# Optimization experiments

Hardware: AMD Instinct MI355X
Metric: run time of the kernel (lower is better)

Reference implementation:

```python
import jax, jax.numpy as jnp
import numpy as np

N = 100000
E = 800000
IN_DIM = 128
HID = 32   # out_channels per head
HEADS = 4
OUT_DIM = 16


def _lin_init(key, fan_in, fan_out):
    k1, k2 = jax.random.split(key)
    bound = 1.0 / np.sqrt(fan_in)
    W = jax.random.uniform(k1, (fan_in, fan_out), minval=-bound, maxval=bound, dtype=jnp.float32)
    b = jax.random.uniform(k2, (fan_out,), minval=-bound, maxval=bound, dtype=jnp.float32)
    return W, b


def setup_inputs() -> dict:
    key = jax.random.key(0)
    keys = jax.random.split(key, 12)
    x = jax.random.normal(keys[0], (N, IN_DIM), dtype=jnp.float32)
    edge_index = jax.random.randint(keys[1], (2, E), 0, N, dtype=jnp.int32)
    inp = {"x": x, "edge_index": edge_index}
    in_dims = [IN_DIM, HID]
    ki = 2
    for l in range(2):
        d_in = in_dims[l]
        Wq, bq = _lin_init(keys[ki], d_in, HEADS * HID); ki += 1
        Wk, bk = _lin_init(keys[ki], d_in, HEADS * HID); ki += 1
        Wv, bv = _lin_init(keys[ki], d_in, HEADS * HID); ki += 1
        Ws, bs = _lin_init(keys[ki], d_in, HID); ki += 1
        inp.update({f"l{l}_Wq": Wq, f"l{l}_bq": bq, f"l{l}_Wk": Wk, f"l{l}_bk": bk,
                    f"l{l}_Wv": Wv, f"l{l}_bv": bv, f"l{l}_Ws": Ws, f"l{l}_bs": bs})
    Wout, bout = _lin_init(keys[ki], HID, OUT_DIM)
    inp["Wout"] = Wout
    inp["bout"] = bout
    return inp


def transformer_conv(x, src, dst, Wq, bq, Wk, bk, Wv, bv, Ws, bs):
    n = x.shape[0]
    q = (x @ Wq + bq).reshape(n, HEADS, HID)  # [N,H,C]
    k = (x @ Wk + bk).reshape(n, HEADS, HID)
    v = (x @ Wv + bv).reshape(n, HEADS, HID)
    scale = 1.0 / np.sqrt(HID)
    # per-edge attention logits over destination neighborhoods
    alpha = jnp.einsum('ehc,ehc->eh', q[dst], k[src]) * scale  # [E,H]
    m = jax.ops.segment_max(alpha, dst, num_segments=n)        # [N,H]
    p = jnp.exp(alpha - m[dst])
    s = jax.ops.segment_sum(p, dst, num_segments=n)            # [N,H]
    a = p / s[dst]                                             # [E,H]
    msg = a[:, :, None] * v[src]                               # [E,H,C]
    agg = jax.ops.segment_sum(msg, dst, num_segments=n)        # [N,H,C]
    # concat=False semantics: mean over heads, plus root/skip linear
    return agg.mean(axis=1) + (x @ Ws + bs)


def reference(x, edge_index,
              l0_Wq, l0_bq, l0_Wk, l0_bk, l0_Wv, l0_bv, l0_Ws, l0_bs,
              l1_Wq, l1_bq, l1_Wk, l1_bk, l1_Wv, l1_bv, l1_Ws, l1_bs,
              Wout, bout):
    src, dst = edge_index[0], edge_index[1]
    h = transformer_conv(x, src, dst, l0_Wq, l0_bq, l0_Wk, l0_bk, l0_Wv, l0_bv, l0_Ws, l0_bs)
    h = jax.nn.relu(h)
    h = transformer_conv(h, src, dst, l1_Wq, l1_bq, l1_Wk, l1_bk, l1_Wv, l1_bv, l1_Ws, l1_bs)
    h = jax.nn.relu(h)
    return h @ Wout + bout
```

## Files before the change

kernel.cpp:

```cpp
#include <hip/hip_runtime.h>
#include <math.h>

#define NN 100000
#define EE 800000
#define IN_DIM 128
#define HID 32
#define HEADS 4
#define QKV 128
#define COLS 416
#define QBH_W 128
#define SB_W 32
#define KV_W 256
#define OUT_DIM 16
#define NTILE 26
#define NBIN 128
#define BINW 782
#define CH 2048
#define NCHUNK 391
#define QSCALE 0.25503512f

typedef __attribute__((ext_vector_type(8))) _Float16 half8;
typedef __attribute__((ext_vector_type(4))) float floatx4;

__device__ __forceinline__ unsigned short f2bf(float f) {
    unsigned int u = __float_as_uint(f);
    unsigned int r = (u + 0x7FFF + ((u >> 16) & 1)) >> 16;
    return (unsigned short)r;
}
__device__ __forceinline__ float bf2f(unsigned short h) {
    return __uint_as_float((unsigned int)h << 16);
}
__device__ __forceinline__ float bf_lo(unsigned int d) {
    return __uint_as_float(d << 16);
}
__device__ __forceinline__ float bf_hi(unsigned int d) {
    return __uint_as_float(d & 0xFFFF0000u);
}
__device__ __forceinline__ unsigned short f2h(float f) {
    _Float16 h = (_Float16)f;
    return __builtin_bit_cast(unsigned short, h);
}

__device__ __forceinline__ void pack_one(
        const float* __restrict__ Wq, const float* __restrict__ Wk,
        const float* __restrict__ Wv, const float* __restrict__ Ws,
        const float* __restrict__ bq, const float* __restrict__ bk,
        const float* __restrict__ bv, const float* __restrict__ bs,
        unsigned short* __restrict__ Wf, float* __restrict__ bp,
        int K, int idx) {
    if (idx < COLS) {
        float b;
        if (idx < 128)      b = bq[idx];
        else if (idx < 256) b = bk[idx - 128];
        else if (idx < 384) b = bv[idx - 256];
        else                b = bs[idx - 384];
        bp[idx] = b;
    }
    int nch = K >> 5;
    if (idx >= nch * NTILE * 64) return;
    int lane = idx & 63;
    int tt = (idx >> 6) % NTILE;
    int c = idx / (NTILE * 64);
    int k0 = c * 32 + (lane >> 4) * 8;
    int col = tt * 16 + (lane & 15);
    #pragma unroll
    for (int j = 0; j < 8; ++j) {
        int k = k0 + j;
        float w;
        if (col < 128)      w = Wq[(size_t)k * 128 + col];
        else if (col < 256) w = Wk[(size_t)k * 128 + (col - 128)];
        else if (col < 384) w = Wv[(size_t)k * 128 + (col - 256)];
        else                w = Ws[(size_t)k * 32 + (col - 384)];
        Wf[(size_t)idx * 8 + j] = f2h(w);
    }
}

__global__ void pack_frag2(
        const float* __restrict__ Wq0, const float* __restrict__ Wk0,
        const float* __restrict__ Wv0, const float* __restrict__ Ws0,
        const float* __restrict__ bq0, const float* __restrict__ bk0,
        const float* __restrict__ bv0, const float* __restrict__ bs0,
        const float* __restrict__ Wq1, const float* __restrict__ Wk1,
        const float* __restrict__ Wv1, const float* __restrict__ Ws1,
        const float* __restrict__ bq1, const float* __restrict__ bk1,
        const float* __restrict__ bv1, const float* __restrict__ bs1,
        unsigned short* __restrict__ Wf0, float* __restrict__ bp0,
        unsigned short* __restrict__ Wf1, float* __restrict__ bp1) {
    const int L0N = 4 * NTILE * 64;
    int gid = blockIdx.x * blockDim.x + threadIdx.x;
    if (gid < L0N) {
        pack_one(Wq0, Wk0, Wv0, Ws0, bq0, bk0, bv0, bs0, Wf0, bp0, 128, gid);
    } else {
        pack_one(Wq1, Wk1, Wv1, Ws1, bq1, bk1, bv1, bs1, Wf1, bp1, 32, gid - L0N);
    }
}


__global__ __launch_bounds__(256) void chunk_hist(
        const int* __restrict__ ei, int* __restrict__ cmat) {
    __shared__ int cnt[NBIN];
    const int t = threadIdx.x;
    const int c = blockIdx.x;
    const int c0 = c * CH;
    const int nc = min(CH, EE - c0);
    if (t < NBIN) cnt[t] = 0;
    __syncthreads();
    for (int i = t; i < nc; i += 256)
        atomicAdd(&cnt[ei[EE + c0 + i] / BINW], 1);
    __syncthreads();
    if (t < NBIN) cmat[c * NBIN + t] = cnt[t];
}

__global__ void btot_scan(const int* __restrict__ cmat, int* __restrict__ bbase) {
    __shared__ int sc[NBIN];
    int b = threadIdx.x;
    int s = 0;
    for (int c = 0; c < NCHUNK; ++c) s += cmat[c * NBIN + b];
    sc[b] = s;
    __syncthreads();
    for (int off = 1; off < NBIN; off <<= 1) {
        int v = (b >= off) ? sc[b - off] : 0;
        __syncthreads();
        sc[b] += v;
        __syncthreads();
    }
    bbase[b] = sc[b] - s;
    if (b == NBIN - 1) bbase[NBIN] = sc[NBIN - 1];
}

__global__ __launch_bounds__(256) void bin_prefix(
        const int* __restrict__ cmat, const int* __restrict__ bbase,
        int* __restrict__ omat) {
    __shared__ int ssum[256];
    const int b = blockIdx.x;
    const int t = threadIdx.x;
    const int bb = bbase[b];
    int c0 = 2 * t;
    int v0 = (c0 < NCHUNK) ? cmat[(size_t)c0 * NBIN + b] : 0;
    int v1 = (c0 + 1 < NCHUNK) ? cmat[(size_t)(c0 + 1) * NBIN + b] : 0;
    int s = v0 + v1;
    ssum[t] = s;
    __syncthreads();
    for (int off = 1; off < 256; off <<= 1) {
        int v = (t >= off) ? ssum[t - off] : 0;
        __syncthreads();
        ssum[t] += v;
        __syncthreads();
    }
    int excl = ssum[t] - s;
    if (c0 < NCHUNK) omat[(size_t)c0 * NBIN + b] = bb + excl;
    if (c0 + 1 < NCHUNK) omat[(size_t)(c0 + 1) * NBIN + b] = bb + excl + v0;
}

__global__ __launch_bounds__(256) void bin_scatter(
        const int* __restrict__ ei, const int* __restrict__ omat,
        int2* __restrict__ pairs) {
    __shared__ int cnt[NBIN], excl[NBIN], cur[NBIN], gbase[NBIN];
    __shared__ int2 stg[CH];
    __shared__ unsigned char binof[CH];
    const int t = threadIdx.x;
    const int c = blockIdx.x;
    const int c0 = c * CH;
    const int nc = min(CH, EE - c0);
    if (t < NBIN) cnt[t] = 0;
    __syncthreads();
    int msrc[8], mdst[8], mbin[8];
    #pragma unroll
    for (int i = 0; i < 8; ++i) {
        int idx = t + i * 256;
        if (idx < nc) {
            msrc[i] = ei[c0 + idx];
            mdst[i] = ei[EE + c0 + idx];
            mbin[i] = mdst[i] / BINW;
            atomicAdd(&cnt[mbin[i]], 1);
        }
    }
    __syncthreads();
    if (t < NBIN) excl[t] = cnt[t];
    __syncthreads();
    for (int off = 1; off < NBIN; off <<= 1) {
        int v = (t < NBIN && t >= off) ? excl[t - off] : 0;
        __syncthreads();
        if (t < NBIN) excl[t] += v;
        __syncthreads();
    }
    if (t < NBIN) {
        int e2 = excl[t] - cnt[t];
        excl[t] = e2; cur[t] = e2;
        gbase[t] = omat[c * NBIN + t];
    }
    __syncthreads();
    #pragma unroll
    for (int i = 0; i < 8; ++i) {
        int idx = t + i * 256;
        if (idx < nc) {
            int pos = atomicAdd(&cur[mbin[i]], 1);
            stg[pos] = make_int2(msrc[i], mdst[i]);
            binof[pos] = (unsigned char)mbin[i];
        }
    }
    __syncthreads();
    for (int i = t; i < nc; i += 256) {
        int b = binof[i];
        pairs[gbase[b] + (i - excl[b])] = stg[i];
    }
}

__global__ __launch_bounds__(256) void bin_sort(
        const int2* __restrict__ pairs, const int* __restrict__ bbase,
        int* __restrict__ roff, int* __restrict__ esrc) {
    __shared__ int hist[BINW + 2];
    __shared__ int ssum[256];
    __shared__ int loc[8192];
    const int b = blockIdx.x;
    const int t = threadIdx.x;
    const int d0 = b * BINW;
    const int nd = (d0 + BINW < NN) ? BINW : (NN - d0);
    const int base = bbase[b];
    const int cnt = bbase[b + 1] - base;
    for (int d = t; d < nd; d += 256) hist[d] = 0;
    __syncthreads();
    for (int i = t; i < cnt; i += 256)
        atomicAdd(&hist[pairs[base + i].y - d0], 1);
    __syncthreads();
    int bi = t * 4;
    int v[4]; int s = 0;
    #pragma unroll
    for (int i = 0; i < 4; ++i) {
        int idx = bi + i;
        v[i] = (idx < nd) ? hist[idx] : 0;
        s += v[i];
    }
    ssum[t] = s;
    __syncthreads();
    for (int off = 1; off < 256; off <<= 1) {
        int val = (t >= off) ? ssum[t - off] : 0;
        __syncthreads();
        ssum[t] += val;
        __syncthreads();
    }
    int run = ssum[t] - s;
    #pragma unroll
    for (int i = 0; i < 4; ++i) {
        int idx = bi + i;
        if (idx < nd) {
            hist[idx] = run;
            roff[d0 + idx] = base + run;
            run += v[i];
        }
    }
    if (b == NBIN - 1 && t == 0) roff[NN] = EE;
    __syncthreads();
    for (int i = t; i < cnt; i += 256) {
        int2 p = pairs[base + i];
        int pos = atomicAdd(&hist[p.y - d0], 1);
        loc[pos] = p.x;
    }
    __syncthreads();
    for (int i = t; i < cnt; i += 256) esrc[base + i] = loc[i];
}

template <int NCH, bool F32>
__global__ __launch_bounds__(256, 3) void gemm_mfma(
        const void* __restrict__ A0,
        const unsigned short* __restrict__ Wf,
        const float* __restrict__ bp, unsigned short* __restrict__ qbh,
        float* __restrict__ sb, unsigned short* __restrict__ kvb) {
    constexpr int K = NCH * 32;
    constexpr int ROWB = 2 * K;
    constexpr int SWZ = (NCH == 4) ? 7 : 3;
    __shared__ char xlds[128 * ROWB];
    __shared__ char olds[4][32][128];
    const int tid = threadIdx.x;
    const int lane = tid & 63;
    const int wv = tid >> 6;
    const int m0b = blockIdx.x << 7;
    const int ml = lane & 15;
    const int quad = lane >> 4;

    if constexpr (F32) {
        const char* X = (const char*)A0;
        const int NPF = 128 * (K / 4);
        for (int p = tid; p < NPF; p += 256) {
            int row = p / (K / 4);
            int pc = p % (K / 4);
            int grow = m0b + row;
            if (grow >= NN) grow = NN - 1;
            float4 v = *(const float4*)(X + (size_t)grow * (4 * K) + pc * 16);
            ushort4 h = {f2h(v.x), f2h(v.y), f2h(v.z), f2h(v.w)};
            int addr = row * ROWB + ((pc * 8) ^ ((row & SWZ) << 4));
            *(ushort4*)(xlds + addr) = h;
        }
    } else {
        const char* X = (const char*)A0;
        const int NP = 128 * ROWB / 16;
        for (int p = tid; p < NP; p += 256) {
            int gb = p * 16;
            int row = gb / ROWB;
            int col = gb & (ROWB - 1);
            int grow = m0b + row;
            if (grow >= NN) grow = NN - 1;
            uint4 d = *(const uint4*)(X + (size_t)grow * ROWB + col);
            *(uint4*)(xlds + row * ROWB + (col ^ ((row & SWZ) << 4))) = d;
        }
    }
    __syncthreads();

    const int m0 = m0b + (wv << 5);
    const int rowL0 = (wv << 5) + ml;
    const int rowL1 = rowL0 + 16;
    char* myl = &olds[wv][0][0];

    for (int g = 0; g < 7; ++g) {
        int tiles[4]; int ntl = 4; int gtype;
        if (g < 2) {
            gtype = 0;
            #pragma unroll
            for (int i = 0; i < 4; ++i) tiles[i] = 4 * g + i;
        } else if (g < 6) {
            gtype = 1;
            int j = g - 2;
            tiles[0] = 8 + 2 * j; tiles[1] = 9 + 2 * j;
            tiles[2] = 16 + 2 * j; tiles[3] = 17 + 2 * j;
        } else {
            gtype = 2; ntl = 2;
            tiles[0] = 24; tiles[1] = 25; tiles[2] = 24; tiles[3] = 25;
        }

        floatx4 acc[2][4] = {};

        #pragma unroll
        for (int c = 0; c < NCH; ++c) {
            int colb = (c * 64 + quad * 16);
            int a0 = rowL0 * ROWB + (colb ^ ((rowL0 & SWZ) << 4));
            int a1 = rowL1 * ROWB + (colb ^ ((rowL1 & SWZ) << 4));
            half8 x0 = *(const half8*)(xlds + a0);
            half8 x1 = *(const half8*)(xlds + a1);
            #pragma unroll
            for (int t = 0; t < 4; ++t) {
                if (t < ntl) {
                    size_t boff = (((size_t)c * NTILE + tiles[t]) * 64 + lane) * 8;
                    half8 w = *(const half8*)(Wf + boff);
                    acc[0][t] = __builtin_amdgcn_mfma_f32_16x16x32_f16(w, x0, acc[0][t], 0, 0, 0);
                    acc[1][t] = __builtin_amdgcn_mfma_f32_16x16x32_f16(w, x1, acc[1][t], 0, 0, 0);
                }
            }
        }

        #pragma unroll
        for (int t = 0; t < 4; ++t) {
            if (t >= ntl) break;
            int tg = tiles[t];
            int c0 = (tg << 4) + (quad << 2);
            float4 b4 = *(const float4*)(bp + c0);
            #pragma unroll
            for (int mt = 0; mt < 2; ++mt) {
                int row = mt * 16 + ml;
                int sz = (row & 7) << 4;
                float v0 = acc[mt][t][0] + b4.x;
                float v1 = acc[mt][t][1] + b4.y;
                float v2 = acc[mt][t][2] + b4.z;
                float v3 = acc[mt][t][3] + b4.w;
                if (gtype == 2) {
                    *(float4*)(myl + row * 128 + ((64 * t + 16 * quad) ^ sz)) =
                        make_float4(v0, v1, v2, v3);
                } else {
                    ushort4 u = {f2bf(v0), f2bf(v1), f2bf(v2), f2bf(v3)};
                    int off;
                    if (gtype == 0) off = 32 * t + 8 * quad;
                    else off = 64 * (t & 1) + 16 * quad + 8 * (t >> 1);
                    *(ushort4*)(myl + row * 128 + (off ^ sz)) = u;
                }
            }
        }

        const int lr = lane >> 3;
        const int lc = (lane & 7) * 16;
        #pragma unroll
        for (int i = 0; i < 4; ++i) {
            int row = i * 8 + lr;
            uint4 d = *(const uint4*)(myl + row * 128 + (lc ^ (lr << 4)));
            int node = m0 + row;
            if (node < NN) {
                char* dst;
                if (gtype == 0)      dst = (char*)qbh + (size_t)node * 256 + g * 128 + lc;
                else if (gtype == 1) dst = (char*)kvb + (size_t)node * 512 + (g - 2) * 128 + lc;
                else                 dst = (char*)sb + (size_t)node * 128 + lc;
                *(uint4*)dst = d;
            }
        }
    }
}

#define ATTN_STEP(u) {                                                       \
    float k0 = bf_lo((u).x), k1 = bf_hi((u).x);                              \
    float k2 = bf_lo((u).y), k3 = bf_hi((u).y);                              \
    float v0 = bf_lo((u).z), v1 = bf_hi((u).z);                              \
    float v2 = bf_lo((u).w), v3 = bf_hi((u).w);                              \
    float part = q4.x * k0 + q4.y * k1 + q4.z * k2 + q4.w * k3;              \
    part += __shfl_xor(part, 1);                                             \
    part += __shfl_xor(part, 2);                                             \
    part += __shfl_xor(part, 4);                                             \
    float p = exp2f(part);                                                   \
    s += p;                                                                  \
    acc.x += p * v0;                                                         \
    acc.y += p * v1;                                                         \
    acc.z += p * v2;                                                         \
    acc.w += p * v3; }

template <bool FINAL>
__global__ __launch_bounds__(256) void fused_attn(
        const unsigned short* __restrict__ qbh, const float* __restrict__ sb,
        const unsigned short* __restrict__ kvb,
        const int* __restrict__ roff, const int* __restrict__ esrc,
        unsigned short* __restrict__ hf,
        const float* __restrict__ Wout, const float* __restrict__ bout,
        float* __restrict__ outp) {
    __shared__ float hbuf[8][32];
    const int tid = threadIdx.x;
    const int lane = tid & 63;
    const int w = (blockIdx.x * blockDim.x + tid) >> 6;
    const int hw = lane >> 5;
    const int n = 2 * w + hw;
    if (n < NN) {
    const int kl = lane & 31;

    ushort4 qu = *(const ushort4*)(qbh + (size_t)n * QBH_W + 4 * kl);
    float4 q4 = make_float4(bf2f(qu.x) * QSCALE, bf2f(qu.y) * QSCALE,
                            bf2f(qu.z) * QSCALE, bf2f(qu.w) * QSCALE);
    float4 sk = *(const float4*)(sb + (size_t)n * SB_W + 4 * (kl & 7));

    float s = 0.f;
    float4 acc = make_float4(0.f, 0.f, 0.f, 0.f);
    const int e0 = roff[n];
    const int cnt = roff[n + 1] - e0;
    int i = 0;
    for (; i + 4 <= cnt; i += 4) {
        int b0 = esrc[e0 + i];
        int b1 = esrc[e0 + i + 1];
        int b2 = esrc[e0 + i + 2];
        int b3 = esrc[e0 + i + 3];
        uint4 u0 = *(const uint4*)(kvb + (size_t)b0 * KV_W + 8 * kl);
        uint4 u1 = *(const uint4*)(kvb + (size_t)b1 * KV_W + 8 * kl);
        uint4 u2 = *(const uint4*)(kvb + (size_t)b2 * KV_W + 8 * kl);
        uint4 u3 = *(const uint4*)(kvb + (size_t)b3 * KV_W + 8 * kl);
        ATTN_STEP(u0); ATTN_STEP(u1); ATTN_STEP(u2); ATTN_STEP(u3);
    }
    for (; i < cnt; ++i) {
        int b0 = esrc[e0 + i];
        uint4 u0 = *(const uint4*)(kvb + (size_t)b0 * KV_W + 8 * kl);
        ATTN_STEP(u0);
    }

    float inv = (s > 0.f) ? 1.f / s : 0.f;
    float4 o;
    o.x = acc.x * inv; o.y = acc.y * inv; o.z = acc.z * inv; o.w = acc.w * inv;
    o.x += __shfl_xor(o.x, 8);  o.y += __shfl_xor(o.y, 8);  o.z += __shfl_xor(o.z, 8);  o.w += __shfl_xor(o.w, 8);
    o.x += __shfl_xor(o.x, 16); o.y += __shfl_xor(o.y, 16); o.z += __shfl_xor(o.z, 16); o.w += __shfl_xor(o.w, 16);
    if (kl < 8) {
        float4 rr;
        rr.x = fmaxf(o.x * 0.25f + sk.x, 0.f);
        rr.y = fmaxf(o.y * 0.25f + sk.y, 0.f);
        rr.z = fmaxf(o.z * 0.25f + sk.z, 0.f);
        rr.w = fmaxf(o.w * 0.25f + sk.w, 0.f);
        int c0 = 4 * kl;
        if constexpr (FINAL) {
            int slot = (tid >> 6) * 2 + hw;
            *(float4*)(&hbuf[slot][c0]) = rr;
        } else {
            ushort4 uh = {f2h(rr.x), f2h(rr.y), f2h(rr.z), f2h(rr.w)};
            *(ushort4*)(hf + (size_t)n * HID + c0) = uh;
        }
    }
    }
    if constexpr (FINAL) {
        __syncthreads();
        if (tid < 128) {
            int slot = tid >> 4;
            int j = tid & 15;
            int n2 = blockIdx.x * 8 + slot;
            if (n2 < NN) {
                float a = bout[j];
                #pragma unroll
                for (int k = 0; k < HID; ++k)
                    a += hbuf[slot][k] * Wout[k * OUT_DIM + j];
                outp[(size_t)n2 * OUT_DIM + j] = a;
            }
        }
    }
}

extern "C" void kernel_launch(void* const* d_in, const int* in_sizes, int n_in,
                              void* d_out, int out_size, void* d_ws, size_t ws_size,
                              hipStream_t stream) {
    const float* x  = (const float*)d_in[0];
    const int*   ei = (const int*)d_in[1];
    const float* l0w[8]; const float* l1w[8];
    for (int i = 0; i < 8; ++i) { l0w[i] = (const float*)d_in[2 + i]; l1w[i] = (const float*)d_in[10 + i]; }
    const float* Wout = (const float*)d_in[18];
    const float* bout = (const float*)d_in[19];
    float* out = (float*)d_out;

    float* ws = (float*)d_ws;
    float* sb   = ws;
    float* bp0  = sb + (size_t)NN * SB_W;
    float* bp1  = bp0 + COLS;
    unsigned short* qbh  = (unsigned short*)(bp1 + COLS);
    unsigned short* kvb  = qbh + (size_t)NN * QBH_W;
    unsigned short* hf   = kvb + (size_t)NN * KV_W;
    unsigned short* Wf0  = hf + (size_t)NN * HID;
    unsigned short* Wf1  = Wf0 + 4 * NTILE * 64 * 8;
    int* ibase  = (int*)(Wf1 + NTILE * 64 * 8);
    int* roff    = ibase;
    int* esrc    = roff + NN + 1;
    int* cmat    = esrc + EE;
    int* omat    = cmat + NCHUNK * NBIN;
    int* bbase   = omat + NCHUNK * NBIN;
    int2* pairs  = (int2*)(bbase + NBIN + 2);

    pack_frag2<<<(5 * NTILE * 64 + 255) / 256, 256, 0, stream>>>(
        l0w[0], l0w[2], l0w[4], l0w[6], l0w[1], l0w[3], l0w[5], l0w[7],
        l1w[0], l1w[2], l1w[4], l1w[6], l1w[1], l1w[3], l1w[5], l1w[7],
        Wf0, bp0, Wf1, bp1);

    chunk_hist<<<NCHUNK, 256, 0, stream>>>(ei, cmat);
    btot_scan<<<1, NBIN, 0, stream>>>(cmat, bbase);
    bin_prefix<<<NBIN, 256, 0, stream>>>(cmat, bbase, omat);
    bin_scatter<<<NCHUNK, 256, 0, stream>>>(ei, omat, pairs);
    bin_sort<<<NBIN, 256, 0, stream>>>(pairs, bbase, roff, esrc);

    const int gemm_blocks = (NN + 127) / 128;
    const int attn_waves = (NN + 1) / 2;
    const int attn_blocks = (attn_waves * 64 + 255) / 256;

    gemm_mfma<4, true><<<gemm_blocks, 256, 0, stream>>>(
        x, Wf0, bp0, qbh, sb, kvb);
    fused_attn<false><<<attn_blocks, 256, 0, stream>>>(
        qbh, sb, kvb, roff, esrc, hf, (const float*)nullptr,
        (const float*)nullptr, (float*)nullptr);

    gemm_mfma<1, false><<<gemm_blocks, 256, 0, stream>>>(
        hf, Wf1, bp1, qbh, sb, kvb);
    fused_attn<true><<<attn_blocks, 256, 0, stream>>>(
        qbh, sb, kvb, roff, esrc, (unsigned short*)nullptr, Wout, bout, out);
}
```

Before: 357.4 us.

## Fuse layer-1 QKV/skip projection into layer-0 attention epilogue

The layer-1 projection (32->416 columns) is now computed inside the layer-0 attention kernel's epilogue from the shared-memory h tile, using fp32 FMAs on 104 threads per 8-node block. This removes the separate layer-1 MFMA GEMM launch and the round trip of the intermediate h through global memory. In exchange it adds a serial 32-step FMA loop to the attention kernel, and it uses double-buffered q/kv/skip workspaces, with the sort scratch aliased onto the second buffers. Nodes past NN are written unguarded in the last block.

```diff
diff --git a/kernel.cpp b/kernel.cpp
--- a/kernel.cpp
+++ b/kernel.cpp
@@ -85,16 +85,35 @@
         const float* __restrict__ bq1, const float* __restrict__ bk1,
         const float* __restrict__ bv1, const float* __restrict__ bs1,
         unsigned short* __restrict__ Wf0, float* __restrict__ bp0,
-        unsigned short* __restrict__ Wf1, float* __restrict__ bp1) {
+        float* __restrict__ w1cat, float* __restrict__ bp1) {
     const int L0N = 4 * NTILE * 64;
     int gid = blockIdx.x * blockDim.x + threadIdx.x;
     if (gid < L0N) {
         pack_one(Wq0, Wk0, Wv0, Ws0, bq0, bk0, bv0, bs0, Wf0, bp0, 128, gid);
-    } else {
-        pack_one(Wq1, Wk1, Wv1, Ws1, bq1, bk1, bv1, bs1, Wf1, bp1, 32, gid - L0N);
-    }
-}
-
+        return;
+    }
+    int g2 = gid - L0N;
+    if (g2 < HID * COLS) {
+        int k = g2 / COLS;
+        int j = g2 - k * COLS;
+        float w;
+        if (j < 128)      w = Wq1[(size_t)k * 128 + j];
+        else if (j < 256) w = Wk1[(size_t)k * 128 + (j - 128)];
+        else if (j < 384) w = Wv1[(size_t)k * 128 + (j - 256)];
+        else              w = Ws1[(size_t)k * 32 + (j - 384)];
+        w1cat[g2] = w;
+        return;
+    }
+    int g3 = g2 - HID * COLS;
+    if (g3 < COLS) {
+        float b;
+        if (g3 < 128)      b = bq1[g3];
+        else if (g3 < 256) b = bk1[g3 - 128];
+        else if (g3 < 384) b = bv1[g3 - 256];
+        else               b = bs1[g3 - 384];
+        bp1[g3] = b;
+    }
+}
 
 __global__ __launch_bounds__(256) void chunk_hist(
         const int* __restrict__ ei, int* __restrict__ cmat) {
@@ -408,14 +427,15 @@
     acc.z += p * v2;                                                         \
     acc.w += p * v3; }
 
-template <bool FINAL>
+template <int MODE>
 __global__ __launch_bounds__(256) void fused_attn(
         const unsigned short* __restrict__ qbh, const float* __restrict__ sb,
         const unsigned short* __restrict__ kvb,
         const int* __restrict__ roff, const int* __restrict__ esrc,
-        unsigned short* __restrict__ hf,
-        const float* __restrict__ Wout, const float* __restrict__ bout,
-        float* __restrict__ outp) {
+        const float* __restrict__ wcat,
+        const float* __restrict__ bvec,
+        unsigned short* __restrict__ qbh2, float* __restrict__ sb2,
+        unsigned short* __restrict__ kvb2, float* __restrict__ outp) {
     __shared__ float hbuf[8][32];
     const int tid = threadIdx.x;
     const int lane = tid & 63;
@@ -423,67 +443,102 @@
     const int hw = lane >> 5;
     const int n = 2 * w + hw;
     if (n < NN) {
-    const int kl = lane & 31;
-
-    ushort4 qu = *(const ushort4*)(qbh + (size_t)n * QBH_W + 4 * kl);
-    float4 q4 = make_float4(bf2f(qu.x) * QSCALE, bf2f(qu.y) * QSCALE,
-                            bf2f(qu.z) * QSCALE, bf2f(qu.w) * QSCALE);
-    float4 sk = *(const float4*)(sb + (size_t)n * SB_W + 4 * (kl & 7));
-
-    float s = 0.f;
-    float4 acc = make_float4(0.f, 0.f, 0.f, 0.f);
-    const int e0 = roff[n];
-    const int cnt = roff[n + 1] - e0;
-    int i = 0;
-    for (; i + 4 <= cnt; i += 4) {
-        int b0 = esrc[e0 + i];
-        int b1 = esrc[e0 + i + 1];
-        int b2 = esrc[e0 + i + 2];
-        int b3 = esrc[e0 + i + 3];
-        uint4 u0 = *(const uint4*)(kvb + (size_t)b0 * KV_W + 8 * kl);
-        uint4 u1 = *(const uint4*)(kvb + (size_t)b1 * KV_W + 8 * kl);
-        uint4 u2 = *(const uint4*)(kvb + (size_t)b2 * KV_W + 8 * kl);
-        uint4 u3 = *(const uint4*)(kvb + (size_t)b3 * KV_W + 8 * kl);
-        ATTN_STEP(u0); ATTN_STEP(u1); ATTN_STEP(u2); ATTN_STEP(u3);
-    }
-    for (; i < cnt; ++i) {
-        int b0 = esrc[e0 + i];
-        uint4 u0 = *(const uint4*)(kvb + (size_t)b0 * KV_W + 8 * kl);
-        ATTN_STEP(u0);
-    }
-
-    float inv = (s > 0.f) ? 1.f / s : 0.f;
-    float4 o;
-    o.x = acc.x * inv; o.y = acc.y * inv; o.z = acc.z * inv; o.w = acc.w * inv;
-    o.x += __shfl_xor(o.x, 8);  o.y += __shfl_xor(o.y, 8);  o.z += __shfl_xor(o.z, 8);  o.w += __shfl_xor(o.w, 8);
-    o.x += __shfl_xor(o.x, 16); o.y += __shfl_xor(o.y, 16); o.z += __shfl_xor(o.z, 16); o.w += __shfl_xor(o.w, 16);
-    if (kl < 8) {
-        float4 rr;
-        rr.x = fmaxf(o.x * 0.25f + sk.x, 0.f);
-        rr.y = fmaxf(o.y * 0.25f + sk.y, 0.f);
-        rr.z = fmaxf(o.z * 0.25f + sk.z, 0.f);
-        rr.w = fmaxf(o.w * 0.25f + sk.w, 0.f);
-        int c0 = 4 * kl;
-        if constexpr (FINAL) {
+        const int kl = lane & 31;
+
+        ushort4 qu = *(const ushort4*)(qbh + (size_t)n * QBH_W + 4 * kl);
+        float4 q4 = make_float4(bf2f(qu.x) * QSCALE, bf2f(qu.y) * QSCALE,
+                                bf2f(qu.z) * QSCALE, bf2f(qu.w) * QSCALE);
+        float4 sk = *(const float4*)(sb + (size_t)n * SB_W + 4 * (kl & 7));
+
+        float s = 0.f;
+        float4 acc = make_float4(0.f, 0.f, 0.f, 0.f);
+        const int e0 = roff[n];
+        const int cnt = roff[n + 1] - e0;
+        int i = 0;
+        for (; i + 4 <= cnt; i += 4) {
+            int b0 = esrc[e0 + i];
+            int b1 = esrc[e0 + i + 1];
+            int b2 = esrc[e0 + i + 2];
+            int b3 = esrc[e0 + i + 3];
+            uint4 u0 = *(const uint4*)(kvb + (size_t)b0 * KV_W + 8 * kl);
+            uint4 u1 = *(const uint4*)(kvb + (size_t)b1 * KV_W + 8 * kl);
+            uint4 u2 = *(const uint4*)(kvb + (size_t)b2 * KV_W + 8 * kl);
+            uint4 u3 = *(const uint4*)(kvb + (size_t)b3 * KV_W + 8 * kl);
+            ATTN_STEP(u0); ATTN_STEP(u1); ATTN_STEP(u2); ATTN_STEP(u3);
+        }
+        for (; i < cnt; ++i) {
+            int b0 = esrc[e0 + i];
+            uint4 u0 = *(const uint4*)(kvb + (size_t)b0 * KV_W + 8 * kl);
+            ATTN_STEP(u0);
+        }
+
+        float inv = (s > 0.f) ? 1.f / s : 0.f;
+        float4 o;
+        o.x = acc.x * inv; o.y = acc.y * inv; o.z = acc.z * inv; o.w = acc.w * inv;
+        o.x += __shfl_xor(o.x, 8);  o.y += __shfl_xor(o.y, 8);  o.z += __shfl_xor(o.z, 8);  o.w += __shfl_xor(o.w, 8);
+        o.x += __shfl_xor(o.x, 16); o.y += __shfl_xor(o.y, 16); o.z += __shfl_xor(o.z, 16); o.w += __shfl_xor(o.w, 16);
+        if (kl < 8) {
+            float4 rr;
+            rr.x = fmaxf(o.x * 0.25f + sk.x, 0.f);
+            rr.y = fmaxf(o.y * 0.25f + sk.y, 0.f);
+            rr.z = fmaxf(o.z * 0.25f + sk.z, 0.f);
+            rr.w = fmaxf(o.w * 0.25f + sk.w, 0.f);
             int slot = (tid >> 6) * 2 + hw;
-            *(float4*)(&hbuf[slot][c0]) = rr;
-        } else {
-            ushort4 uh = {f2h(rr.x), f2h(rr.y), f2h(rr.z), f2h(rr.w)};
-            *(ushort4*)(hf + (size_t)n * HID + c0) = uh;
-        }
-    }
-    }
-    if constexpr (FINAL) {
-        __syncthreads();
+            *(float4*)(&hbuf[slot][4 * kl]) = rr;
+        }
+    }
+    __syncthreads();
+
+    if constexpr (MODE == 0) {
+        if (tid < 104) {
+            const int c = 4 * tid;
+            float4 b4 = *(const float4*)(bvec + c);
+            float4 a8[8];
+            #pragma unroll
+            for (int s2 = 0; s2 < 8; ++s2) a8[s2] = b4;
+            for (int k = 0; k < HID; ++k) {
+                float4 w4 = *(const float4*)(wcat + (size_t)k * COLS + c);
+                #pragma unroll
+                for (int s2 = 0; s2 < 8; ++s2) {
+                    float hv = hbuf[s2][k];
+                    a8[s2].x += hv * w4.x; a8[s2].y += hv * w4.y;
+                    a8[s2].z += hv * w4.z; a8[s2].w += hv * w4.w;
+                }
+            }
+            const int nb = blockIdx.x * 8;
+            #pragma unroll
+            for (int s2 = 0; s2 < 8; ++s2) {
+                int n2 = nb + s2;
+                if (c < 128) {
+                    ushort4 u = {f2bf(a8[s2].x), f2bf(a8[s2].y),
+                                 f2bf(a8[s2].z), f2bf(a8[s2].w)};
+                    *(ushort4*)(qbh2 + (size_t)n2 * QBH_W + c) = u;
+                } else if (c < 256) {
+                    int cc = c - 128;
+                    ushort4 u = {f2bf(a8[s2].x), f2bf(a8[s2].y),
+                                 f2bf(a8[s2].z), f2bf(a8[s2].w)};
+                    *(ushort4*)(kvb2 + (size_t)n2 * KV_W + 2 * cc) = u;
+                } else if (c < 384) {
+                    int cc = c - 256;
+                    ushort4 u = {f2bf(a8[s2].x), f2bf(a8[s2].y),
+                                 f2bf(a8[s2].z), f2bf(a8[s2].w)};
+                    *(ushort4*)(kvb2 + (size_t)n2 * KV_W + 2 * cc + 4) = u;
+                } else {
+                    *(float4*)(sb2 + (size_t)n2 * SB_W + (c - 384)) =
+                        make_float4(a8[s2].x, a8[s2].y, a8[s2].z, a8[s2].w);
+                }
+            }
+        }
+    } else {
         if (tid < 128) {
             int slot = tid >> 4;
             int j = tid & 15;
             int n2 = blockIdx.x * 8 + slot;
             if (n2 < NN) {
-                float a = bout[j];
+                float a = bvec[j];
                 #pragma unroll
                 for (int k = 0; k < HID; ++k)
-                    a += hbuf[slot][k] * Wout[k * OUT_DIM + j];
+                    a += hbuf[slot][k] * wcat[k * OUT_DIM + j];
                 outp[(size_t)n2 * OUT_DIM + j] = a;
             }
         }
@@ -502,26 +557,28 @@
     float* out = (float*)d_out;
 
     float* ws = (float*)d_ws;
-    float* sb   = ws;
-    float* bp0  = sb + (size_t)NN * SB_W;
-    float* bp1  = bp0 + COLS;
-    unsigned short* qbh  = (unsigned short*)(bp1 + COLS);
+    float* sb    = ws;
+    float* sb2   = sb + (size_t)NN * SB_W;
+    float* bp0   = sb2 + (size_t)NN * SB_W;
+    float* bp1   = bp0 + COLS;
+    float* w1cat = bp1 + COLS;
+    unsigned short* qbh  = (unsigned short*)(w1cat + HID * COLS);
     unsigned short* kvb  = qbh + (size_t)NN * QBH_W;
-    unsigned short* hf   = kvb + (size_t)NN * KV_W;
-    unsigned short* Wf0  = hf + (size_t)NN * HID;
-    unsigned short* Wf1  = Wf0 + 4 * NTILE * 64 * 8;
-    int* ibase  = (int*)(Wf1 + NTILE * 64 * 8);
-    int* roff    = ibase;
-    int* esrc    = roff + NN + 1;
-    int* cmat    = esrc + EE;
-    int* omat    = cmat + NCHUNK * NBIN;
-    int* bbase   = omat + NCHUNK * NBIN;
-    int2* pairs  = (int2*)(bbase + NBIN + 2);
-
-    pack_frag2<<<(5 * NTILE * 64 + 255) / 256, 256, 0, stream>>>(
+    unsigned short* qbh2 = kvb + (size_t)NN * KV_W;
+    unsigned short* kvb2 = qbh2 + (size_t)NN * QBH_W;
+    unsigned short* Wf0  = kvb2 + (size_t)NN * KV_W;
+    int* roff  = (int*)(Wf0 + 4 * NTILE * 64 * 8);
+    int* esrc  = roff + NN + 1;
+    int* bbase = esrc + EE;
+    int2* pairs = (int2*)qbh2;
+    int* cmat   = (int*)kvb2;
+    int* omat   = cmat + NCHUNK * NBIN;
+
+    const int packN = 4 * NTILE * 64 + HID * COLS + COLS;
+    pack_frag2<<<(packN + 255) / 256, 256, 0, stream>>>(
         l0w[0], l0w[2], l0w[4], l0w[6], l0w[1], l0w[3], l0w[5], l0w[7],
         l1w[0], l1w[2], l1w[4], l1w[6], l1w[1], l1w[3], l1w[5], l1w[7],
-        Wf0, bp0, Wf1, bp1);
+        Wf0, bp0, w1cat, bp1);
 
     chunk_hist<<<NCHUNK, 256, 0, stream>>>(ei, cmat);
     btot_scan<<<1, NBIN, 0, stream>>>(cmat, bbase);
@@ -530,17 +587,13 @@
     bin_sort<<<NBIN, 256, 0, stream>>>(pairs, bbase, roff, esrc);
 
     const int gemm_blocks = (NN + 127) / 128;
-    const int attn_waves = (NN + 1) / 2;
-    const int attn_blocks = (attn_waves * 64 + 255) / 256;
+    const int attn_blocks = ((NN + 1) / 2 * 64 + 255) / 256;
 
     gemm_mfma<4, true><<<gemm_blocks, 256, 0, stream>>>(
         x, Wf0, bp0, qbh, sb, kvb);
-    fused_attn<false><<<attn_blocks, 256, 0, stream>>>(
-        qbh, sb, kvb, roff, esrc, hf, (const float*)nullptr,
-        (const float*)nullptr, (float*)nullptr);
-
-    gemm_mfma<1, false><<<gemm_blocks, 256, 0, stream>>>(
-        hf, Wf1, bp1, qbh, sb, kvb);
-    fused_attn<true><<<attn_blocks, 256, 0, stream>>>(
-        qbh, sb, kvb, roff, esrc, (unsigned short*)nullptr, Wout, bout, out);
-}
+    fused_attn<0><<<attn_blocks, 256, 0, stream>>>(
+        qbh, sb, kvb, roff, esrc, w1cat, bp1, qbh2, sb2, kvb2, (float*)nullptr);
+    fused_attn<1><<<attn_blocks, 256, 0, stream>>>(
+        qbh2, sb2, kvb2, roff, esrc, Wout, bout,
+        (unsigned short*)nullptr, (float*)nullptr, (unsigned short*)nullptr, out);
+}
```

New measurement: 398.4 us. 1.11x slower.

## Reorder bin scan to drop serial chunk sum; add LDS-free K=32 GEMM

Applied to the files above, without the earlier changes.

The single-block scan that summed all 391 chunk counts per bin serially is replaced: bin_prefix now produces per-bin relative offsets and totals, a tiny scan turns the totals into bin bases, and bin_scatter adds the base. The layer-1 GEMM with K=32 gets a dedicated kernel that loads its input fragments straight from global memory into registers, skipping the LDS staging and barrier. Both changes cut fixed overhead in small stages, at the cost of an extra buffer and a duplicated GEMM epilogue.

```diff
diff --git a/kernel.cpp b/kernel.cpp
--- a/kernel.cpp
+++ b/kernel.cpp
@@ -111,30 +111,12 @@
     if (t < NBIN) cmat[c * NBIN + t] = cnt[t];
 }
 
-__global__ void btot_scan(const int* __restrict__ cmat, int* __restrict__ bbase) {
-    __shared__ int sc[NBIN];
-    int b = threadIdx.x;
-    int s = 0;
-    for (int c = 0; c < NCHUNK; ++c) s += cmat[c * NBIN + b];
-    sc[b] = s;
-    __syncthreads();
-    for (int off = 1; off < NBIN; off <<= 1) {
-        int v = (b >= off) ? sc[b - off] : 0;
-        __syncthreads();
-        sc[b] += v;
-        __syncthreads();
-    }
-    bbase[b] = sc[b] - s;
-    if (b == NBIN - 1) bbase[NBIN] = sc[NBIN - 1];
-}
-
 __global__ __launch_bounds__(256) void bin_prefix(
-        const int* __restrict__ cmat, const int* __restrict__ bbase,
-        int* __restrict__ omat) {
+        const int* __restrict__ cmat, int* __restrict__ omat,
+        int* __restrict__ btot) {
     __shared__ int ssum[256];
     const int b = blockIdx.x;
     const int t = threadIdx.x;
-    const int bb = bbase[b];
     int c0 = 2 * t;
     int v0 = (c0 < NCHUNK) ? cmat[(size_t)c0 * NBIN + b] : 0;
     int v1 = (c0 + 1 < NCHUNK) ? cmat[(size_t)(c0 + 1) * NBIN + b] : 0;
@@ -148,13 +130,30 @@
         __syncthreads();
     }
     int excl = ssum[t] - s;
-    if (c0 < NCHUNK) omat[(size_t)c0 * NBIN + b] = bb + excl;
-    if (c0 + 1 < NCHUNK) omat[(size_t)(c0 + 1) * NBIN + b] = bb + excl + v0;
+    if (c0 < NCHUNK) omat[(size_t)c0 * NBIN + b] = excl;
+    if (c0 + 1 < NCHUNK) omat[(size_t)(c0 + 1) * NBIN + b] = excl + v0;
+    if (t == 255) btot[b] = ssum[255];
+}
+
+__global__ void btot_scan2(const int* __restrict__ btot, int* __restrict__ bbase) {
+    __shared__ int sc[NBIN];
+    int b = threadIdx.x;
+    int s = btot[b];
+    sc[b] = s;
+    __syncthreads();
+    for (int off = 1; off < NBIN; off <<= 1) {
+        int v = (b >= off) ? sc[b - off] : 0;
+        __syncthreads();
+        sc[b] += v;
+        __syncthreads();
+    }
+    bbase[b] = sc[b] - s;
+    if (b == NBIN - 1) bbase[NBIN] = sc[NBIN - 1];
 }
 
 __global__ __launch_bounds__(256) void bin_scatter(
         const int* __restrict__ ei, const int* __restrict__ omat,
-        int2* __restrict__ pairs) {
+        const int* __restrict__ bbase, int2* __restrict__ pairs) {
     __shared__ int cnt[NBIN], excl[NBIN], cur[NBIN], gbase[NBIN];
     __shared__ int2 stg[CH];
     __shared__ unsigned char binof[CH];
@@ -187,7 +186,7 @@
     if (t < NBIN) {
         int e2 = excl[t] - cnt[t];
         excl[t] = e2; cur[t] = e2;
-        gbase[t] = omat[c * NBIN + t];
+        gbase[t] = bbase[t] + omat[c * NBIN + t];
     }
     __syncthreads();
     #pragma unroll
@@ -260,15 +259,15 @@
     for (int i = t; i < cnt; i += 256) esrc[base + i] = loc[i];
 }
 
-template <int NCH, bool F32>
-__global__ __launch_bounds__(256, 3) void gemm_mfma(
-        const void* __restrict__ A0,
+__global__ __launch_bounds__(256, 3) void gemm_mfma4(
+        const float* __restrict__ X,
         const unsigned short* __restrict__ Wf,
         const float* __restrict__ bp, unsigned short* __restrict__ qbh,
         float* __restrict__ sb, unsigned short* __restrict__ kvb) {
+    constexpr int NCH = 4;
     constexpr int K = NCH * 32;
     constexpr int ROWB = 2 * K;
-    constexpr int SWZ = (NCH == 4) ? 7 : 3;
+    constexpr int SWZ = 7;
     __shared__ char xlds[128 * ROWB];
     __shared__ char olds[4][32][128];
     const int tid = threadIdx.x;
@@ -278,30 +277,17 @@
     const int ml = lane & 15;
     const int quad = lane >> 4;
 
-    if constexpr (F32) {
-        const char* X = (const char*)A0;
+    {
         const int NPF = 128 * (K / 4);
         for (int p = tid; p < NPF; p += 256) {
             int row = p / (K / 4);
             int pc = p % (K / 4);
             int grow = m0b + row;
             if (grow >= NN) grow = NN - 1;
-            float4 v = *(const float4*)(X + (size_t)grow * (4 * K) + pc * 16);
+            float4 v = *(const float4*)((const char*)X + (size_t)grow * (4 * K) + pc * 16);
             ushort4 h = {f2h(v.x), f2h(v.y), f2h(v.z), f2h(v.w)};
             int addr = row * ROWB + ((pc * 8) ^ ((row & SWZ) << 4));
             *(ushort4*)(xlds + addr) = h;
-        }
-    } else {
-        const char* X = (const char*)A0;
-        const int NP = 128 * ROWB / 16;
-        for (int p = tid; p < NP; p += 256) {
-            int gb = p * 16;
-            int row = gb / ROWB;
-            int col = gb & (ROWB - 1);
-            int grow = m0b + row;
-            if (grow >= NN) grow = NN - 1;
-            uint4 d = *(const uint4*)(X + (size_t)grow * ROWB + col);
-            *(uint4*)(xlds + row * ROWB + (col ^ ((row & SWZ) << 4))) = d;
         }
     }
     __syncthreads();
@@ -392,6 +378,97 @@
     }
 }
 
+__global__ __launch_bounds__(256) void gemm_small(
+        const unsigned short* __restrict__ hf,
+        const unsigned short* __restrict__ Wf,
+        const float* __restrict__ bp, unsigned short* __restrict__ qbh,
+        float* __restrict__ sb, unsigned short* __restrict__ kvb) {
+    __shared__ char olds[4][32][128];
+    const int tid = threadIdx.x;
+    const int lane = tid & 63;
+    const int wv = tid >> 6;
+    const int m0 = (blockIdx.x << 7) + (wv << 5);
+    const int ml = lane & 15;
+    const int quad = lane >> 4;
+    char* myl = &olds[wv][0][0];
+
+    int r0 = m0 + ml;       if (r0 >= NN) r0 = NN - 1;
+    int r1 = m0 + 16 + ml;  if (r1 >= NN) r1 = NN - 1;
+    half8 x0 = *(const half8*)(hf + (size_t)r0 * HID + quad * 8);
+    half8 x1 = *(const half8*)(hf + (size_t)r1 * HID + quad * 8);
+
+    for (int g = 0; g < 7; ++g) {
+        int tiles[4]; int ntl = 4; int gtype;
+        if (g < 2) {
+            gtype = 0;
+            #pragma unroll
+            for (int i = 0; i < 4; ++i) tiles[i] = 4 * g + i;
+        } else if (g < 6) {
+            gtype = 1;
+            int j = g - 2;
+            tiles[0] = 8 + 2 * j; tiles[1] = 9 + 2 * j;
+            tiles[2] = 16 + 2 * j; tiles[3] = 17 + 2 * j;
+        } else {
+            gtype = 2; ntl = 2;
+            tiles[0] = 24; tiles[1] = 25; tiles[2] = 24; tiles[3] = 25;
+        }
+
+        floatx4 acc[2][4] = {};
+        #pragma unroll
+        for (int t = 0; t < 4; ++t) {
+            if (t < ntl) {
+                size_t boff = ((size_t)tiles[t] * 64 + lane) * 8;
+                half8 w = *(const half8*)(Wf + boff);
+                acc[0][t] = __builtin_amdgcn_mfma_f32_16x16x32_f16(w, x0, acc[0][t], 0, 0, 0);
+                acc[1][t] = __builtin_amdgcn_mfma_f32_16x16x32_f16(w, x1, acc[1][t], 0, 0, 0);
+            }
+        }
+
+        #pragma unroll
+        for (int t = 0; t < 4; ++t) {
+            if (t >= ntl) break;
+            int tg = tiles[t];
+            int c0 = (tg << 4) + (quad << 2);
+            float4 b4 = *(const float4*)(bp + c0);
+            #pragma unroll
+            for (int mt = 0; mt < 2; ++mt) {
+                int row = mt * 16 + ml;
+                int sz = (row & 7) << 4;
+                float v0 = acc[mt][t][0] + b4.x;
+                float v1 = acc[mt][t][1] + b4.y;
+                float v2 = acc[mt][t][2] + b4.z;
+                float v3 = acc[mt][t][3] + b4.w;
+                if (gtype == 2) {
+                    *(float4*)(myl + row * 128 + ((64 * t + 16 * quad) ^ sz)) =
+                        make_float4(v0, v1, v2, v3);
+                } else {
+                    ushort4 u = {f2bf(v0), f2bf(v1), f2bf(v2), f2bf(v3)};
+                    int off;
+                    if (gtype == 0) off = 32 * t + 8 * quad;
+                    else off = 64 * (t & 1) + 16 * quad + 8 * (t >> 1);
+                    *(ushort4*)(myl + row * 128 + (off ^ sz)) = u;
+                }
+            }
+        }
+
+        const int lr = lane >> 3;
+        const int lc = (lane & 7) * 16;
+        #pragma unroll
+        for (int i = 0; i < 4; ++i) {
+            int row = i * 8 + lr;
+            uint4 d = *(const uint4*)(myl + row * 128 + (lc ^ (lr << 4)));
+            int node = m0 + row;
+            if (node < NN) {
+                char* dst;
+                if (gtype == 0)      dst = (char*)qbh + (size_t)node * 256 + g * 128 + lc;
+                else if (gtype == 1) dst = (char*)kvb + (size_t)node * 512 + (g - 2) * 128 + lc;
+                else                 dst = (char*)sb + (size_t)node * 128 + lc;
+                *(uint4*)dst = d;
+            }
+        }
+    }
+}
+
 #define ATTN_STEP(u) {                                                       \
     float k0 = bf_lo((u).x), k1 = bf_hi((u).x);                              \
     float k2 = bf_lo((u).y), k3 = bf_hi((u).y);                              \
@@ -516,7 +593,8 @@
     int* cmat    = esrc + EE;
     int* omat    = cmat + NCHUNK * NBIN;
     int* bbase   = omat + NCHUNK * NBIN;
-    int2* pairs  = (int2*)(bbase + NBIN + 2);
+    int* btot    = bbase + NBIN + 2;
+    int2* pairs  = (int2*)(btot + NBIN);
 
     pack_frag2<<<(5 * NTILE * 64 + 255) / 256, 256, 0, stream>>>(
         l0w[0], l0w[2], l0w[4], l0w[6], l0w[1], l0w[3], l0w[5], l0w[7],
@@ -524,23 +602,20 @@
         Wf0, bp0, Wf1, bp1);
 
     chunk_hist<<<NCHUNK, 256, 0, stream>>>(ei, cmat);
-    btot_scan<<<1, NBIN, 0, stream>>>(cmat, bbase);
-    bin_prefix<<<NBIN, 256, 0, stream>>>(cmat, bbase, omat);
-    bin_scatter<<<NCHUNK, 256, 0, stream>>>(ei, omat, pairs);
+    bin_prefix<<<NBIN, 256, 0, stream>>>(cmat, omat, btot);
+    btot_scan2<<<1, NBIN, 0, stream>>>(btot, bbase);
+    bin_scatter<<<NCHUNK, 256, 0, stream>>>(ei, omat, bbase, pairs);
     bin_sort<<<NBIN, 256, 0, stream>>>(pairs, bbase, roff, esrc);
 
     const int gemm_blocks = (NN + 127) / 128;
-    const int attn_waves = (NN + 1) / 2;
-    const int attn_blocks = (attn_waves * 64 + 255) / 256;
-
-    gemm_mfma<4, true><<<gemm_blocks, 256, 0, stream>>>(
-        x, Wf0, bp0, qbh, sb, kvb);
+    const int attn_blocks = ((NN + 1) / 2 * 64 + 255) / 256;
+
+    gemm_mfma4<<<gemm_blocks, 256, 0, stream>>>(x, Wf0, bp0, qbh, sb, kvb);
     fused_attn<false><<<attn_blocks, 256, 0, stream>>>(
         qbh, sb, kvb, roff, esrc, hf, (const float*)nullptr,
         (const float*)nullptr, (float*)nullptr);
 
-    gemm_mfma<1, false><<<gemm_blocks, 256, 0, stream>>>(
-        hf, Wf1, bp1, qbh, sb, kvb);
+    gemm_small<<<gemm_blocks, 256, 0, stream>>>(hf, Wf1, bp1, qbh, sb, kvb);
     fused_attn<true><<<attn_blocks, 256, 0, stream>>>(
         qbh, sb, kvb, roff, esrc, (unsigned short*)nullptr, Wout, bout, out);
 }
```

After: 342.6 us. 1.04x faster.
